# Optimization experiments

Measured on AMD Instinct MI355X. Metric: run time of the kernel, lower is better.

Reference implementation:

```python
import jax, jax.numpy as jnp
import numpy as np

PILLAR_SIZE = 0.075
PC_RANGE = (-54.0, -54.0, -5.0, 54.0, 54.0, 3.0)
H = round((PC_RANGE[4] - PC_RANGE[1]) / PILLAR_SIZE)  # 1440
W = round((PC_RANGE[3] - PC_RANGE[0]) / PILLAR_SIZE)  # 1440
X_OFFSET = PILLAR_SIZE / 2.0 + PC_RANGE[0]
Y_OFFSET = PILLAR_SIZE / 2.0 + PC_RANGE[1]
BATCH = 4
N_PER_BATCH = 500_000
C_FEAT = 16


def setup_inputs() -> dict:
    key = jax.random.key(0)
    k1, k2, k3 = jax.random.split(key, 3)
    N = BATCH * N_PER_BATCH
    # integer pillar-grid coordinates (x, y) of each point
    pts_xy = jax.random.randint(k1, (N, 2), 0, W, dtype=jnp.int32)
    pts_batch_cnt = jnp.full((BATCH,), N_PER_BATCH, dtype=jnp.int32)
    feats = jax.random.normal(k2, (N, C_FEAT), dtype=jnp.float32)
    # first two channels are the absolute xy coordinates of the points
    base = jnp.array([PC_RANGE[0], PC_RANGE[1]], dtype=jnp.float32)
    xy = (pts_xy.astype(jnp.float32) * PILLAR_SIZE + base
          + jax.random.uniform(k3, (N, 2), dtype=jnp.float32) * PILLAR_SIZE)
    feats = feats.at[:, :2].set(xy)
    return {"pts_xy": pts_xy, "pts_batch_cnt": pts_batch_cnt, "pts_features": feats}


def reference(pts_xy, pts_batch_cnt, pts_features):
    batch = pts_batch_cnt.shape[0]
    N = pts_xy.shape[0]
    # batch index of each point from the per-batch counts
    batch_idx = jnp.repeat(jnp.arange(batch, dtype=jnp.int32), pts_batch_cnt,
                           total_repeat_length=N)
    x = pts_xy[:, 0].astype(jnp.int32)
    y = pts_xy[:, 1].astype(jnp.int32)
    # flat pillar id per point: (b, y, x) -> b*H*W + y*W + x  (== point_pillar_index)
    flat = (batch_idx * H + y) * W + x
    # scatter: mark occupied pillars
    mask = jnp.zeros((batch * H * W,), dtype=bool).at[flat].set(True)
    # cumsum compaction: rank of each occupied pillar (row-major order), -1 elsewhere
    csum = jnp.cumsum(mask.astype(jnp.int32))
    positions = jnp.where(mask, csum - 1, -1)
    # indices of active pillars (sorted flat order == compaction order)
    active = jnp.nonzero(mask)[0]                      # (P,) data-dependent size
    b = (active // (H * W)).astype(jnp.int32)
    rem = active % (H * W)
    hy = (rem // W).astype(jnp.int32)
    wx = (rem % W).astype(jnp.int32)
    pillar_indices = jnp.stack([b, hy, wx], axis=1)    # (P, 3) [batch, y, x]
    # compact pillar index per point
    point_pillar_indices = positions[flat]             # (N,)
    # pillar centers in world coords, gathered back to points
    pillar_centers = jnp.stack([wx.astype(jnp.float32) * PILLAR_SIZE + X_OFFSET,
                                hy.astype(jnp.float32) * PILLAR_SIZE + Y_OFFSET],
                               axis=1)                 # (P, 2)
    point_pillar_centers = pts_features[:, :2] - pillar_centers[point_pillar_indices]
    point_pillar_features = jnp.concatenate([point_pillar_centers, pts_features], axis=1)
    return pillar_indices, point_pillar_indices, point_pillar_features
```

## Files before the change

kernel.cpp:

```cpp
#include <hip/hip_runtime.h>

namespace {

typedef float f32x4 __attribute__((ext_vector_type(4)));

constexpr int   HG  = 1440;
constexpr int   WG  = 1440;
constexpr int   HWG = HG * WG;
constexpr float PIL = 0.075f;
constexpr float XOFF = (float)(0.075 / 2.0 - 54.0);
constexpr float YOFF = XOFF;

constexpr int SCAN_T    = 256;
constexpr int SCAN_WPT  = 4;
constexpr int SCAN_CHUNK = SCAN_T * SCAN_WPT;

__device__ inline unsigned nib4(unsigned u) {
    return (u * 0x01020408u) >> 24 & 0xFu;
}
__device__ inline unsigned pack_word(uint4 a, uint4 b) {
    return  nib4(a.x)        | nib4(a.y) << 4  | nib4(a.z) << 8  | nib4(a.w) << 12
          | nib4(b.x) << 16  | nib4(b.y) << 20 | nib4(b.z) << 24 | nib4(b.w) << 28;
}

__global__ __launch_bounds__(256) void pqag_scatter(
    const int* __restrict__ xy, const int* __restrict__ cnt, int batch, int N,
    unsigned char* __restrict__ bytemap)
{
    int i = blockIdx.x * 256 + threadIdx.x;
    if (i >= N) return;
    int2 p = reinterpret_cast<const int2*>(xy)[i];
    int b = 0, acc = 0;
    for (int k = 0; k < batch - 1; ++k) { acc += cnt[k]; b += (i >= acc) ? 1 : 0; }
    int flat = (b * HG + p.y) * WG + p.x;
    bytemap[flat] = 1;
}

__global__ __launch_bounds__(SCAN_T) void pqag_scan_a(
    const unsigned char* __restrict__ bytemap, int nwords,
    unsigned int* __restrict__ bsums)
{
    int t = threadIdx.x;
    int wbase = blockIdx.x * SCAN_CHUNK + t * SCAN_WPT;
    unsigned int s = 0;
    if (wbase + SCAN_WPT <= nwords) {
        const uint4* q = reinterpret_cast<const uint4*>(bytemap) + 2ll * wbase;
#pragma unroll
        for (int k = 0; k < 2 * SCAN_WPT; ++k) {
            uint4 v = q[k];
            s += __popc(v.x) + __popc(v.y) + __popc(v.z) + __popc(v.w);
        }
    } else {
        for (int w = wbase; w < nwords && w < wbase + SCAN_WPT; ++w)
            for (int j = 0; j < 32; ++j) s += bytemap[32 * w + j];
    }
#pragma unroll
    for (int d = 32; d > 0; d >>= 1) s += __shfl_down(s, d);
    __shared__ unsigned int red[SCAN_T / 64];
    if ((t & 63) == 0) red[t >> 6] = s;
    __syncthreads();
    if (t == 0) {
        unsigned int tot = 0;
        for (int w = 0; w < SCAN_T / 64; ++w) tot += red[w];
        bsums[blockIdx.x] = tot;
    }
}

__global__ __launch_bounds__(SCAN_T) void pqag_scan_b(unsigned int* bsums, int nb)
{
    int t = threadIdx.x;
    unsigned int v = (t < nb) ? bsums[t] : 0u;
    unsigned int x = v;
#pragma unroll
    for (int d = 1; d < 64; d <<= 1) {
        unsigned int y = __shfl_up(x, d);
        if ((t & 63) >= d) x += y;
    }
    __shared__ unsigned int ws[SCAN_T / 64];
    if ((t & 63) == 63) ws[t >> 6] = x;
    __syncthreads();
    unsigned int off = 0;
    for (int w = 0; w < (t >> 6); ++w) off += ws[w];
    if (t < nb) bsums[t] = off + x - v;
}

__global__ __launch_bounds__(SCAN_T) void pqag_scan_c(
    const unsigned char* __restrict__ bytemap, int nwords,
    const unsigned int* __restrict__ bsums,
    unsigned int* __restrict__ bits,
    unsigned int* __restrict__ wordscan)
{
    int t = threadIdx.x;
    int wbase = blockIdx.x * SCAN_CHUNK + t * SCAN_WPT;
    unsigned int w[SCAN_WPT];
    if (wbase + SCAN_WPT <= nwords) {
        const uint4* q = reinterpret_cast<const uint4*>(bytemap) + 2ll * wbase;
#pragma unroll
        for (int k = 0; k < SCAN_WPT; ++k)
            w[k] = pack_word(q[2 * k], q[2 * k + 1]);
    } else {
        for (int k = 0; k < SCAN_WPT; ++k) {
            unsigned int wv = 0;
            if (wbase + k < nwords)
                for (int j = 0; j < 32; ++j)
                    wv |= (unsigned)(bytemap[32 * (wbase + k) + j]) << j;
            w[k] = wv;
        }
    }
    unsigned int s = 0;
#pragma unroll
    for (int k = 0; k < SCAN_WPT; ++k) s += __popc(w[k]);
    unsigned int x = s;
#pragma unroll
    for (int d = 1; d < 64; d <<= 1) {
        unsigned int y = __shfl_up(x, d);
        if ((t & 63) >= d) x += y;
    }
    __shared__ unsigned int ws[SCAN_T / 64];
    if ((t & 63) == 63) ws[t >> 6] = x;
    __syncthreads();
    unsigned int run = bsums[blockIdx.x] + x - s;
    for (int wv = 0; wv < (t >> 6); ++wv) run += ws[wv];
#pragma unroll
    for (int k = 0; k < SCAN_WPT; ++k) {
        int widx = wbase + k;
        if (widx >= nwords) break;
        bits[widx]     = w[k];
        wordscan[widx] = run;
        run += __popc(w[k]);
    }
}

__global__ __launch_bounds__(256) void pqag_emit(
    const unsigned int* __restrict__ bits,
    const unsigned int* __restrict__ wordscan, int ncells,
    float* __restrict__ pillar_out)
{
    int cell = blockIdx.x * 256 + threadIdx.x;
    if (cell >= ncells) return;
    unsigned int word = bits[cell >> 5];
    int bit = cell & 31;
    if ((word >> bit) & 1u) {
        unsigned int pid = wordscan[cell >> 5] + __popc(word & ((1u << bit) - 1u));
        int bidx = cell / HWG;
        int rem  = cell - bidx * HWG;
        int hy   = rem / WG;
        int wx   = rem - hy * WG;
        float* row = pillar_out + 3ull * pid;
        __builtin_nontemporal_store((float)bidx, row + 0);
        __builtin_nontemporal_store((float)hy,   row + 1);
        __builtin_nontemporal_store((float)wx,   row + 2);
    }
}

constexpr int PT_T = 256;
__global__ __launch_bounds__(PT_T) void pqag_point(
    const int* __restrict__ xy, const int* __restrict__ cnt, int batch,
    const float* __restrict__ feats, int N,
    const unsigned int* __restrict__ bits,
    const unsigned int* __restrict__ wordscan,
    float* __restrict__ ppi_out, float* __restrict__ feat_out)
{
    __shared__ float lds[PT_T][19];
    int t = threadIdx.x;
    int blockBase = blockIdx.x * PT_T;
    int i = blockBase + t;
    int nvalid = N - blockBase; if (nvalid > PT_T) nvalid = PT_T;

    if (t < nvalid) {
        int2 p = reinterpret_cast<const int2*>(xy)[i];
        int b = 0, acc = 0;
        for (int k = 0; k < batch - 1; ++k) { acc += cnt[k]; b += (i >= acc) ? 1 : 0; }
        int flat = (b * HG + p.y) * WG + p.x;
        int widx = flat >> 5, bit = flat & 31;
        unsigned int pid = wordscan[widx] + __popc(bits[widx] & ((1u << bit) - 1u));
        __builtin_nontemporal_store((float)pid, ppi_out + i);

        const f32x4* fr = reinterpret_cast<const f32x4*>(feats + 16ll * i);
        f32x4 f0 = __builtin_nontemporal_load(fr + 0);
        f32x4 f1 = __builtin_nontemporal_load(fr + 1);
        f32x4 f2 = __builtin_nontemporal_load(fr + 2);
        f32x4 f3 = __builtin_nontemporal_load(fr + 3);
        float cx = (float)p.x * PIL + XOFF;
        float cy = (float)p.y * PIL + YOFF;
        lds[t][0]  = f0.x - cx;  lds[t][1]  = f0.y - cy;
        lds[t][2]  = f0.x;  lds[t][3]  = f0.y;  lds[t][4]  = f0.z;  lds[t][5]  = f0.w;
        lds[t][6]  = f1.x;  lds[t][7]  = f1.y;  lds[t][8]  = f1.z;  lds[t][9]  = f1.w;
        lds[t][10] = f2.x;  lds[t][11] = f2.y;  lds[t][12] = f2.z;  lds[t][13] = f2.w;
        lds[t][14] = f3.x;  lds[t][15] = f3.y;  lds[t][16] = f3.z;  lds[t][17] = f3.w;
    }
    __syncthreads();

    float* dst = feat_out + 18ll * blockBase;
    int total = nvalid * 18;
    for (int j = t; j < total; j += PT_T) {
        int p = j / 18;
        int c = j - p * 18;
        __builtin_nontemporal_store(lds[p][c], dst + j);
    }
}

}

extern "C" void kernel_launch(void* const* d_in, const int* in_sizes, int n_in,
                              void* d_out, int out_size, void* d_ws, size_t ws_size,
                              hipStream_t stream)
{
    const int*   xy    = (const int*)d_in[0];
    const int*   cnt   = (const int*)d_in[1];
    const float* feats = (const float*)d_in[2];

    int N     = in_sizes[0] / 2;
    int batch = in_sizes[1];
    int ncells = batch * HWG;
    int nwords = ncells / 32;
    long long P = (out_size - 19ll * N) / 3;

    unsigned char* bytemap  = (unsigned char*)d_ws;
    unsigned int*  bits     = (unsigned int*)(bytemap + ncells);
    unsigned int*  wordscan = bits + nwords;
    unsigned int*  bsums    = wordscan + nwords;

    float* pillar_out = (float*)d_out;
    float* ppi_out    = pillar_out + 3ll * P;
    float* feat_out   = ppi_out + N;

    (void)hipMemsetAsync(bytemap, 0, (size_t)ncells, stream);

    int nb_pts = (N + 255) / 256;
    pqag_scatter<<<nb_pts, 256, 0, stream>>>(xy, cnt, batch, N, bytemap);

    int nb_scan = (nwords + SCAN_CHUNK - 1) / SCAN_CHUNK;
    pqag_scan_a<<<nb_scan, SCAN_T, 0, stream>>>(bytemap, nwords, bsums);
    pqag_scan_b<<<1, SCAN_T, 0, stream>>>(bsums, nb_scan);
    pqag_scan_c<<<nb_scan, SCAN_T, 0, stream>>>(bytemap, nwords, bsums, bits, wordscan);

    int nb_emit = (ncells + 255) / 256;
    pqag_emit<<<nb_emit, 256, 0, stream>>>(bits, wordscan, ncells, pillar_out);

    pqag_point<<<nb_pts, PT_T, 0, stream>>>(xy, cnt, batch, feats, N, bits, wordscan,
                                            ppi_out, feat_out);
}
```

Measured before the change: 357.7 us.

## Fuse scan-offset into scan_c and pillar emit into point kernel

Drops the single-block scan_b kernel: each scan_c block now redoes the scan of block sums itself in its first wavefront and picks out its own offset. The pillar emit kernel is folded into the point kernel as a grid-stride loop over cells, cutting the launch count from six kernels to four. The LDS staging buffer is now unpadded so rows can be written back as 16-byte vector nontemporal stores when the output is aligned. The byte counting also changes to test bytes equal to 1 with a bit trick, which adds ALU work to every scan word and raises LDS bank conflicts on the row writes.

```diff
diff --git a/kernel.cpp b/kernel.cpp
--- a/kernel.cpp
+++ b/kernel.cpp
@@ -15,8 +15,12 @@
 constexpr int SCAN_WPT  = 4;
 constexpr int SCAN_CHUNK = SCAN_T * SCAN_WPT;
 
-__device__ inline unsigned nib4(unsigned u) {
-    return (u * 0x01020408u) >> 24 & 0xFu;
+__device__ inline unsigned eq1_msb(unsigned w) {
+    unsigned t1 = (w & 0x7F7F7F7Fu) ^ 0x01010101u;
+    return ~((t1 + 0x7F7F7F7Fu) | t1 | w) & 0x80808080u;
+}
+__device__ inline unsigned nib4(unsigned w) {
+    return (((eq1_msb(w) >> 7) * 0x01020408u) >> 24) & 0xFu;
 }
 __device__ inline unsigned pack_word(uint4 a, uint4 b) {
     return  nib4(a.x)        | nib4(a.y) << 4  | nib4(a.z) << 8  | nib4(a.w) << 12
@@ -48,11 +52,12 @@
 #pragma unroll
         for (int k = 0; k < 2 * SCAN_WPT; ++k) {
             uint4 v = q[k];
-            s += __popc(v.x) + __popc(v.y) + __popc(v.z) + __popc(v.w);
+            s += __popc(eq1_msb(v.x)) + __popc(eq1_msb(v.y))
+               + __popc(eq1_msb(v.z)) + __popc(eq1_msb(v.w));
         }
     } else {
         for (int w = wbase; w < nwords && w < wbase + SCAN_WPT; ++w)
-            for (int j = 0; j < 32; ++j) s += bytemap[32 * w + j];
+            for (int j = 0; j < 32; ++j) s += (bytemap[32 * w + j] == 1);
     }
 #pragma unroll
     for (int d = 32; d > 0; d >>= 1) s += __shfl_down(s, d);
@@ -66,31 +71,37 @@
     }
 }
 
-__global__ __launch_bounds__(SCAN_T) void pqag_scan_b(unsigned int* bsums, int nb)
-{
-    int t = threadIdx.x;
-    unsigned int v = (t < nb) ? bsums[t] : 0u;
-    unsigned int x = v;
-#pragma unroll
-    for (int d = 1; d < 64; d <<= 1) {
-        unsigned int y = __shfl_up(x, d);
-        if ((t & 63) >= d) x += y;
-    }
-    __shared__ unsigned int ws[SCAN_T / 64];
-    if ((t & 63) == 63) ws[t >> 6] = x;
-    __syncthreads();
-    unsigned int off = 0;
-    for (int w = 0; w < (t >> 6); ++w) off += ws[w];
-    if (t < nb) bsums[t] = off + x - v;
-}
-
-__global__ __launch_bounds__(SCAN_T) void pqag_scan_c(
+__global__ __launch_bounds__(SCAN_T) void pqag_scan_cb(
     const unsigned char* __restrict__ bytemap, int nwords,
-    const unsigned int* __restrict__ bsums,
+    const unsigned int* __restrict__ bsums, int nb,
     unsigned int* __restrict__ bits,
     unsigned int* __restrict__ wordscan)
 {
     int t = threadIdx.x;
+    __shared__ unsigned int sblk;
+    __shared__ unsigned int ws[SCAN_T / 64];
+
+    if (t < 64) {
+        int base4 = t * 4;
+        unsigned int b[4];
+#pragma unroll
+        for (int k = 0; k < 4; ++k)
+            b[k] = (base4 + k < nb) ? bsums[base4 + k] : 0u;
+        unsigned int tot = b[0] + b[1] + b[2] + b[3];
+        unsigned int inc = tot;
+#pragma unroll
+        for (int d = 1; d < 64; d <<= 1) {
+            unsigned int y = __shfl_up(inc, d);
+            if (t >= d) inc += y;
+        }
+        unsigned int excl = inc - tot;
+        if (t == (blockIdx.x >> 2)) {
+            unsigned int v = excl;
+            for (int k = 0; k < (blockIdx.x & 3); ++k) v += b[k];
+            sblk = v;
+        }
+    }
+
     int wbase = blockIdx.x * SCAN_CHUNK + t * SCAN_WPT;
     unsigned int w[SCAN_WPT];
     if (wbase + SCAN_WPT <= nwords) {
@@ -103,7 +114,7 @@
             unsigned int wv = 0;
             if (wbase + k < nwords)
                 for (int j = 0; j < 32; ++j)
-                    wv |= (unsigned)(bytemap[32 * (wbase + k) + j]) << j;
+                    wv |= (unsigned)(bytemap[32 * (wbase + k) + j] == 1) << j;
             w[k] = wv;
         }
     }
@@ -116,10 +127,9 @@
         unsigned int y = __shfl_up(x, d);
         if ((t & 63) >= d) x += y;
     }
-    __shared__ unsigned int ws[SCAN_T / 64];
     if ((t & 63) == 63) ws[t >> 6] = x;
     __syncthreads();
-    unsigned int run = bsums[blockIdx.x] + x - s;
+    unsigned int run = sblk + x - s;
     for (int wv = 0; wv < (t >> 6); ++wv) run += ws[wv];
 #pragma unroll
     for (int k = 0; k < SCAN_WPT; ++k) {
@@ -131,37 +141,16 @@
     }
 }
 
-__global__ __launch_bounds__(256) void pqag_emit(
-    const unsigned int* __restrict__ bits,
-    const unsigned int* __restrict__ wordscan, int ncells,
-    float* __restrict__ pillar_out)
-{
-    int cell = blockIdx.x * 256 + threadIdx.x;
-    if (cell >= ncells) return;
-    unsigned int word = bits[cell >> 5];
-    int bit = cell & 31;
-    if ((word >> bit) & 1u) {
-        unsigned int pid = wordscan[cell >> 5] + __popc(word & ((1u << bit) - 1u));
-        int bidx = cell / HWG;
-        int rem  = cell - bidx * HWG;
-        int hy   = rem / WG;
-        int wx   = rem - hy * WG;
-        float* row = pillar_out + 3ull * pid;
-        __builtin_nontemporal_store((float)bidx, row + 0);
-        __builtin_nontemporal_store((float)hy,   row + 1);
-        __builtin_nontemporal_store((float)wx,   row + 2);
-    }
-}
-
 constexpr int PT_T = 256;
-__global__ __launch_bounds__(PT_T) void pqag_point(
+__global__ __launch_bounds__(PT_T) void pqag_point_emit(
     const int* __restrict__ xy, const int* __restrict__ cnt, int batch,
     const float* __restrict__ feats, int N,
     const unsigned int* __restrict__ bits,
     const unsigned int* __restrict__ wordscan,
-    float* __restrict__ ppi_out, float* __restrict__ feat_out)
-{
-    __shared__ float lds[PT_T][19];
+    float* __restrict__ ppi_out, float* __restrict__ feat_out, int aligned16,
+    int ncells, float* __restrict__ pillar_out)
+{
+    __shared__ float lds[PT_T * 18];
     int t = threadIdx.x;
     int blockBase = blockIdx.x * PT_T;
     int i = blockBase + t;
@@ -183,20 +172,45 @@
         f32x4 f3 = __builtin_nontemporal_load(fr + 3);
         float cx = (float)p.x * PIL + XOFF;
         float cy = (float)p.y * PIL + YOFF;
-        lds[t][0]  = f0.x - cx;  lds[t][1]  = f0.y - cy;
-        lds[t][2]  = f0.x;  lds[t][3]  = f0.y;  lds[t][4]  = f0.z;  lds[t][5]  = f0.w;
-        lds[t][6]  = f1.x;  lds[t][7]  = f1.y;  lds[t][8]  = f1.z;  lds[t][9]  = f1.w;
-        lds[t][10] = f2.x;  lds[t][11] = f2.y;  lds[t][12] = f2.z;  lds[t][13] = f2.w;
-        lds[t][14] = f3.x;  lds[t][15] = f3.y;  lds[t][16] = f3.z;  lds[t][17] = f3.w;
+        float* r = &lds[t * 18];
+        r[0]  = f0.x - cx;  r[1]  = f0.y - cy;
+        r[2]  = f0.x;  r[3]  = f0.y;  r[4]  = f0.z;  r[5]  = f0.w;
+        r[6]  = f1.x;  r[7]  = f1.y;  r[8]  = f1.z;  r[9]  = f1.w;
+        r[10] = f2.x;  r[11] = f2.y;  r[12] = f2.z;  r[13] = f2.w;
+        r[14] = f3.x;  r[15] = f3.y;  r[16] = f3.z;  r[17] = f3.w;
     }
     __syncthreads();
 
     float* dst = feat_out + 18ll * blockBase;
     int total = nvalid * 18;
-    for (int j = t; j < total; j += PT_T) {
-        int p = j / 18;
-        int c = j - p * 18;
-        __builtin_nontemporal_store(lds[p][c], dst + j);
+    if (aligned16) {
+        int nq = total >> 2;
+        for (int j = t; j < nq; j += PT_T) {
+            f32x4 v = *reinterpret_cast<f32x4*>(&lds[4 * j]);
+            __builtin_nontemporal_store(v, reinterpret_cast<f32x4*>(dst) + j);
+        }
+        for (int j = (nq << 2) + t; j < total; j += PT_T)
+            __builtin_nontemporal_store(lds[j], dst + j);
+    } else {
+        for (int j = t; j < total; j += PT_T)
+            __builtin_nontemporal_store(lds[j], dst + j);
+    }
+
+    int stride = gridDim.x * PT_T;
+    for (int cell = blockBase + t; cell < ncells; cell += stride) {
+        unsigned int word = bits[cell >> 5];
+        int bit = cell & 31;
+        if ((word >> bit) & 1u) {
+            unsigned int pid = wordscan[cell >> 5] + __popc(word & ((1u << bit) - 1u));
+            int bidx = cell / HWG;
+            int rem  = cell - bidx * HWG;
+            int hy   = rem / WG;
+            int wx   = rem - hy * WG;
+            float* row = pillar_out + 3ull * pid;
+            __builtin_nontemporal_store((float)bidx, row + 0);
+            __builtin_nontemporal_store((float)hy,   row + 1);
+            __builtin_nontemporal_store((float)wx,   row + 2);
+        }
     }
 }
 
@@ -224,6 +238,7 @@
     float* pillar_out = (float*)d_out;
     float* ppi_out    = pillar_out + 3ll * P;
     float* feat_out   = ppi_out + N;
+    int aligned16 = (((3ll * P + N) & 3) == 0) ? 1 : 0;
 
     (void)hipMemsetAsync(bytemap, 0, (size_t)ncells, stream);
 
@@ -232,12 +247,10 @@
 
     int nb_scan = (nwords + SCAN_CHUNK - 1) / SCAN_CHUNK;
     pqag_scan_a<<<nb_scan, SCAN_T, 0, stream>>>(bytemap, nwords, bsums);
-    pqag_scan_b<<<1, SCAN_T, 0, stream>>>(bsums, nb_scan);
-    pqag_scan_c<<<nb_scan, SCAN_T, 0, stream>>>(bytemap, nwords, bsums, bits, wordscan);
-
-    int nb_emit = (ncells + 255) / 256;
-    pqag_emit<<<nb_emit, 256, 0, stream>>>(bits, wordscan, ncells, pillar_out);
-
-    pqag_point<<<nb_pts, PT_T, 0, stream>>>(xy, cnt, batch, feats, N, bits, wordscan,
-                                            ppi_out, feat_out);
-}
+    pqag_scan_cb<<<nb_scan, SCAN_T, 0, stream>>>(bytemap, nwords, bsums, nb_scan,
+                                                 bits, wordscan);
+
+    pqag_point_emit<<<nb_pts, PT_T, 0, stream>>>(xy, cnt, batch, feats, N,
+                                                 bits, wordscan, ppi_out, feat_out,
+                                                 aligned16, ncells, pillar_out);
+}
```

New measurement: 337.5 us. -5.6%, faster.
